# Kernel optimization log

Measured on AMD Instinct MI355X. Metric: run time of the kernel, lower is better.

Reference implementation:

```python
import jax, jax.numpy as jnp
import numpy as np

B, S, E, H = 32, 512, 512, 8
D = E // H  # head dim = 64
EPS = 1e-5


def setup_inputs() -> dict:
    key = jax.random.key(0)
    ks = jax.random.split(key, 6)
    x = jax.random.normal(ks[0], (B, S, E), dtype=jnp.float32)
    # nn.MultiheadAttention packed in-projection: [3E, E] weight, [3E] bias
    w_in = jax.random.normal(ks[1], (3 * E, E), dtype=jnp.float32) * 0.02
    b_in = jnp.zeros((3 * E,), dtype=jnp.float32)
    # out_proj: Linear(E, E)
    w_out = jax.random.normal(ks[2], (E, E), dtype=jnp.float32) * 0.02
    b_out = jnp.zeros((E,), dtype=jnp.float32)
    # LayerNorm(E) affine params
    gamma = jnp.ones((E,), dtype=jnp.float32)
    beta = jnp.zeros((E,), dtype=jnp.float32)
    return {"x": x, "w_in": w_in, "b_in": b_in, "w_out": w_out,
            "b_out": b_out, "gamma": gamma, "beta": beta}


def reference(x, w_in, b_in, w_out, b_out, gamma, beta):
    b, s, e = x.shape
    # packed QKV projection (torch: x @ W^T + b)
    qkv = x @ w_in.T + b_in                      # [B, S, 3E]
    q, k, v = jnp.split(qkv, 3, axis=-1)         # each [B, S, E]
    def to_heads(t):
        return t.reshape(b, s, H, D).transpose(0, 2, 1, 3)  # [B, H, S, D]
    q, k, v = to_heads(q), to_heads(k), to_heads(v)
    scores = jnp.einsum("bhqd,bhkd->bhqk", q, k) / jnp.sqrt(jnp.float32(D))
    att_w = jax.nn.softmax(scores, axis=-1)      # [B, H, S, S] per-head weights
    z = jnp.einsum("bhqk,bhkd->bhqd", att_w, v)  # [B, H, S, D]
    z = z.transpose(0, 2, 1, 3).reshape(b, s, e) # merge heads
    z = z @ w_out.T + b_out                      # out projection
    z = z + x                                    # residual connection
    # LayerNorm over last dim
    mu = jnp.mean(z, axis=-1, keepdims=True)
    var = jnp.var(z, axis=-1, keepdims=True)
    y = (z - mu) * jax.lax.rsqrt(var + EPS) * gamma + beta
    return (y, att_w)
```

## Files before the change

kernel.cpp:

```cpp
#include <hip/hip_runtime.h>
#include <hip/hip_bf16.h>
#include <stdint.h>

#define Bb 32
#define Ss 512
#define Ee 512
#define Hh 8
#define Dd 64
#define EPSf 1e-5f

typedef __attribute__((ext_vector_type(8))) unsigned short ushort8_t;
typedef __attribute__((ext_vector_type(4))) unsigned short ushort4_t;
typedef __attribute__((ext_vector_type(4))) float f32x4;
typedef __attribute__((ext_vector_type(4))) unsigned int uint4_t;
typedef __attribute__((ext_vector_type(8))) __bf16 bf16x8;

union U8cast { ushort8_t u; bf16x8 b; uint4_t w; };
__device__ __forceinline__ bf16x8 as_bf16x8(ushort8_t u) { U8cast c; c.u = u; return c.b; }
__device__ __forceinline__ bf16x8 words_bf16x8(unsigned int w0, unsigned int w1,
                                               unsigned int w2, unsigned int w3) {
  U8cast c; c.w = (uint4_t){w0, w1, w2, w3}; return c.b;
}

__device__ __forceinline__ unsigned short f2bf(float f) {
  __bf16 b = (__bf16)f;
  return __builtin_bit_cast(unsigned short, b);
}
__device__ __forceinline__ unsigned int pack2bf(float lo, float hi) {
  return ((unsigned int)f2bf(hi) << 16) | f2bf(lo);
}

__device__ __forceinline__ f32x4 mfma16(bf16x8 a, bf16x8 b, f32x4 c) {
  return __builtin_amdgcn_mfma_f32_16x16x32_bf16(a, b, c, 0, 0, 0);
}

__device__ __forceinline__ void async16(const unsigned short* g, unsigned short* l) {
  __builtin_amdgcn_global_load_lds(
      (const __attribute__((address_space(1))) void*)g,
      (__attribute__((address_space(3))) void*)l, 16, 0, 0);
}

__global__ __launch_bounds__(256) void cvt_all(
    const float* __restrict__ x, const float* __restrict__ win,
    const float* __restrict__ wout, unsigned short* __restrict__ dst) {
  const int NX = 1048576;
  const int NW = 98304;
  const int NT = NX + NW + 32768;
  int i = blockIdx.x * 256 + threadIdx.x;
  int stride = gridDim.x * 256;
  for (; i < NT; i += stride) {
    const float* s;
    int off;
    if (i < NX) { s = x; off = i; }
    else if (i < NX + NW) { s = win; off = i - NX; }
    else { s = wout; off = i - NX - NW; }
    float4 v0 = ((const float4*)s)[2 * off];
    float4 v1 = ((const float4*)s)[2 * off + 1];
    ushort8_t o;
    o[0] = f2bf(v0.x); o[1] = f2bf(v0.y); o[2] = f2bf(v0.z); o[3] = f2bf(v0.w);
    o[4] = f2bf(v1.x); o[5] = f2bf(v1.y); o[6] = f2bf(v1.z); o[7] = f2bf(v1.w);
    ((ushort8_t*)dst)[i] = o;
  }
}

__global__ __launch_bounds__(256) void qkv_mm(
    const unsigned short* __restrict__ Xb, const unsigned short* __restrict__ Wb,
    const float* __restrict__ bin,
    unsigned short* __restrict__ QL, unsigned short* __restrict__ KL,
    unsigned short* __restrict__ VL) {
  __shared__ unsigned short SH[128 * 128];
  unsigned short* As = SH;
  unsigned short* Bs = SH + 128 * 64;
  const int tid = threadIdx.x;
  const int w = tid >> 6, l = tid & 63;
  const int lr = l & 15, lg = l >> 4;
  const int id = blockIdx.x;
  const int gid = (id & 7) * 192 + (id >> 3);
  const int bx = gid % 12, by = gid / 12;
  const int m0 = by * 128, n0 = bx * 128;
  const int wm = (w >> 1) * 64, wn = (w & 1) * 64;
  f32x4 acc[4][4];
#pragma unroll
  for (int i = 0; i < 4; ++i)
#pragma unroll
    for (int j = 0; j < 4; ++j) acc[i][j] = (f32x4){0.f, 0.f, 0.f, 0.f};

  for (int k0 = 0; k0 < 512; k0 += 64) {
#pragma unroll
    for (int i = 0; i < 4; ++i) {
      int ci = (w * 4 + i) * 64 + l;
      int row = ci >> 3, kc = ci & 7;
      int gkc = kc ^ (row & 7);
      async16(Xb + (size_t)(m0 + row) * 512 + k0 + gkc * 8, &As[(w * 4 + i) * 512]);
      async16(Wb + (size_t)(n0 + row) * 512 + k0 + gkc * 8, &Bs[(w * 4 + i) * 512]);
    }
    __syncthreads();
#pragma unroll
    for (int ks = 0; ks < 2; ++ks) {
      bf16x8 af[4], bfr[4];
#pragma unroll
      for (int mf = 0; mf < 4; ++mf) {
        int row = wm + mf * 16 + lr;
        int gc = ks * 4 + lg;
        af[mf] = as_bf16x8(*(const ushort8_t*)&As[row * 64 + ((gc ^ (row & 7)) * 8)]);
      }
#pragma unroll
      for (int nf = 0; nf < 4; ++nf) {
        int row = wn + nf * 16 + lr;
        int gc = ks * 4 + lg;
        bfr[nf] = as_bf16x8(*(const ushort8_t*)&Bs[row * 64 + ((gc ^ (row & 7)) * 8)]);
      }
#pragma unroll
      for (int mf = 0; mf < 4; ++mf)
#pragma unroll
        for (int nf = 0; nf < 4; ++nf) acc[mf][nf] = mfma16(af[mf], bfr[nf], acc[mf][nf]);
    }
    __syncthreads();
  }

  const int which = n0 >> 9;
  const int bb = m0 >> 9, s0b = m0 & 511;
  const int h0 = (n0 & 511) >> 6;
#pragma unroll
  for (int nf = 0; nf < 4; ++nf) {
    int nl = wn + nf * 16 + lr;
    float bias = bin[n0 + nl];
#pragma unroll
    for (int mf = 0; mf < 4; ++mf) {
#pragma unroll
      for (int r = 0; r < 4; ++r) {
        int ml = wm + mf * 16 + lg * 4 + r;
        int row = (which == 2) ? nl : ml;
        int col = (which == 2) ? ml : nl;
        SH[row * 128 + ((((col >> 3) ^ (row & 7)) << 3) | (col & 7))] =
            f2bf(acc[mf][nf][r] + bias);
      }
    }
  }
  __syncthreads();

  unsigned short* dst = (which == 0) ? QL : (which == 1) ? KL : VL;
  const int frag0 = s0b >> 3;
#pragma unroll
  for (int i = 0; i < 8; ++i) {
    int c = tid + i * 256;
    int h_rel = c >> 10, cc = c & 1023;
    int fr = cc >> 6, ln = cc & 63;
    int row, col;
    if (which == 0) {
      row = (fr >> 1) * 16 + (ln & 15);
      col = h_rel * 64 + (fr & 1) * 32 + (ln >> 4) * 8;
    } else if (which == 1) {
      row = (fr >> 2) * 32 + ((fr >> 1) & 1) * 4 + ((ln & 15) >> 2) * 8 + (ln & 3);
      col = h_rel * 64 + (fr & 1) * 32 + (ln >> 4) * 8;
    } else {
      row = h_rel * 64 + (fr & 3) * 16 + (ln & 15);
      col = (fr >> 2) * 32 + (ln >> 4) * 8;
    }
    ushort8_t v = *(const ushort8_t*)&SH[row * 128 + (((col >> 3) ^ (row & 7)) << 3)];
    size_t base = (size_t)(bb * Hh + h0 + h_rel) * 32768;
    *(ushort8_t*)&dst[base + (size_t)(frag0 + fr) * 512 + ln * 8] = v;
  }
}

__global__ __launch_bounds__(512, 4) void attn_fused(
    const unsigned short* __restrict__ QL, const unsigned short* __restrict__ KL,
    const unsigned short* __restrict__ VL, float* __restrict__ att,
    unsigned short* __restrict__ Zb) {
  __shared__ unsigned short SH[2][8192];
  unsigned short* KB = &SH[0][0];
  const int tid = threadIdx.x;
  const int w = tid >> 6, l = tid & 63;
  const int lr = l & 15, lg = l >> 4;
  const int id = blockIdx.x;
  const int bh = (id >> 5) * 8 + (id & 7);
  const int m0 = ((id >> 3) & 3) * 128;
  const int b = bh >> 3, h = bh & 7;
  const unsigned short* Qp = QL + (size_t)bh * 32768;
  const unsigned short* Kp = KL + (size_t)bh * 32768;
  const unsigned short* Vp = VL + (size_t)bh * 32768;

  const int qb = (m0 >> 4) + w;
  bf16x8 bq0 = as_bf16x8(*(const ushort8_t*)(Qp + (size_t)(qb * 2) * 512 + l * 8));
  bf16x8 bq1 = as_bf16x8(*(const ushort8_t*)(Qp + (size_t)(qb * 2 + 1) * 512 + l * 8));

#define STAGE_K4(C)                                                            \
  async16(Kp + (size_t)(C)*4096 + w * 512 + l * 8,                             \
          &KB[((C) & 3) * 4096 + w * 512]);
#define STAGE_K(C, buf)                                                        \
  async16(Kp + (size_t)(C)*4096 + w * 512 + l * 8, &SH[buf][w * 512]);
#define STAGE_V(C, buf)                                                        \
  async16(Vp + (size_t)(C)*4096 + w * 512 + l * 8, &SH[buf][4096 + w * 512]);

  float ssum = 0.f;
  STAGE_K4(0);
  STAGE_K4(1);
  STAGE_K4(2);
#pragma unroll
  for (int C = 0; C < 8; ++C) {
    if (C <= 5) {
      asm volatile("s_waitcnt vmcnt(2)" ::: "memory");
    } else if (C == 6) {
      asm volatile("s_waitcnt vmcnt(1)" ::: "memory");
    } else {
      asm volatile("s_waitcnt vmcnt(0)" ::: "memory");
    }
    __builtin_amdgcn_s_barrier();
    if (C < 5) STAGE_K4(C + 3);
    f32x4 s4[4];
#pragma unroll
    for (int j = 0; j < 4; ++j) {
      bf16x8 ak0 = as_bf16x8(*(const ushort8_t*)&KB[(C & 3) * 4096 + (2 * j) * 512 + l * 8]);
      bf16x8 ak1 = as_bf16x8(*(const ushort8_t*)&KB[(C & 3) * 4096 + (2 * j + 1) * 512 + l * 8]);
      f32x4 z = (f32x4){0.f, 0.f, 0.f, 0.f};
      z = mfma16(ak0, bq0, z);
      s4[j] = mfma16(ak1, bq1, z);
    }
#pragma unroll
    for (int j = 0; j < 4; ++j) {
      float p0 = __expf(s4[j][0] * 0.125f);
      float p1 = __expf(s4[j][1] * 0.125f);
      float p2 = __expf(s4[j][2] * 0.125f);
      float p3 = __expf(s4[j][3] * 0.125f);
      ssum += (p0 + p1) + (p2 + p3);
    }
  }
  ssum += __shfl_xor(ssum, 16);
  ssum += __shfl_xor(ssum, 32);
  const float inv = 1.0f / ssum;
  __builtin_amdgcn_s_barrier();

  f32x4 o[4];
#pragma unroll
  for (int df = 0; df < 4; ++df) o[df] = (f32x4){0.f, 0.f, 0.f, 0.f};
  float* attb = att + (size_t)bh * Ss * Ss + (size_t)(m0 + w * 16) * Ss;
  const int dr8 = l >> 3, dc = l & 7;
  const int src0 = ((dc >> 1) << 4) + dr8;
  const int podd = dc & 1;

  STAGE_K(0, 0);
  STAGE_V(0, 0);
  __syncthreads();
#pragma unroll
  for (int C = 0; C < 8; ++C) {
    if (C < 7) {
      STAGE_K(C + 1, (C + 1) & 1);
      STAGE_V(C + 1, (C + 1) & 1);
    }
    f32x4 s4[4];
#pragma unroll
    for (int j = 0; j < 4; ++j) {
      bf16x8 ak0 = as_bf16x8(*(const ushort8_t*)&SH[C & 1][(2 * j) * 512 + l * 8]);
      bf16x8 ak1 = as_bf16x8(*(const ushort8_t*)&SH[C & 1][(2 * j + 1) * 512 + l * 8]);
      f32x4 z = (f32x4){0.f, 0.f, 0.f, 0.f};
      z = mfma16(ak0, bq0, z);
      s4[j] = mfma16(ak1, bq1, z);
    }
#pragma unroll
    for (int j = 0; j < 4; ++j)
#pragma unroll
      for (int r = 0; r < 4; ++r)
        s4[j][r] = __expf(s4[j][r] * 0.125f) * inv;

#pragma unroll
    for (int cc = 0; cc < 2; ++cc) {
      int c2 = 2 * C + cc;
#pragma unroll
      for (int hh = 0; hh < 2; ++hh) {
        int srcl = src0 + hh * 8;
        f32x4 g;
        g[0] = __shfl(s4[2 * cc + podd][0], srcl, 64);
        g[1] = __shfl(s4[2 * cc + podd][1], srcl, 64);
        g[2] = __shfl(s4[2 * cc + podd][2], srcl, 64);
        g[3] = __shfl(s4[2 * cc + podd][3], srcl, 64);
        float* p = attb + (size_t)(hh * 8 + dr8) * Ss + c2 * 32 + dc * 4;
        __builtin_nontemporal_store(g, (f32x4*)p);
      }
      bf16x8 bp = words_bf16x8(pack2bf(s4[2 * cc][0], s4[2 * cc][1]),
                               pack2bf(s4[2 * cc][2], s4[2 * cc][3]),
                               pack2bf(s4[2 * cc + 1][0], s4[2 * cc + 1][1]),
                               pack2bf(s4[2 * cc + 1][2], s4[2 * cc + 1][3]));
#pragma unroll
      for (int df = 0; df < 4; ++df) {
        bf16x8 av = as_bf16x8(
            *(const ushort8_t*)&SH[C & 1][4096 + (cc * 4 + df) * 512 + l * 8]);
        o[df] = mfma16(av, bp, o[df]);
      }
    }
    if (C < 7) {
      asm volatile("s_waitcnt vmcnt(4)" ::: "memory");
      __builtin_amdgcn_s_barrier();
    }
  }

  unsigned short* zrow = Zb + ((size_t)(b * Ss) + m0 + w * 16 + lr) * Ee + h * Dd;
#pragma unroll
  for (int df = 0; df < 4; ++df) {
    ushort4_t zz;
    zz[0] = f2bf(o[df][0]); zz[1] = f2bf(o[df][1]);
    zz[2] = f2bf(o[df][2]); zz[3] = f2bf(o[df][3]);
    *(ushort4_t*)(zrow + df * 16 + lg * 4) = zz;
  }
#undef STAGE_K4
#undef STAGE_K
#undef STAGE_V
}

__global__ __launch_bounds__(256) void out_ln(
    const unsigned short* __restrict__ Zb, const unsigned short* __restrict__ Wb,
    const float* __restrict__ bout, const float* __restrict__ X,
    const float* __restrict__ gamma, const float* __restrict__ beta,
    float* __restrict__ Y) {
  __shared__ unsigned short As[32 * 32];
  __shared__ unsigned short Bs[512 * 32];
  const int tid = threadIdx.x;
  const int w = tid >> 6, l = tid & 63;
  const int lr = l & 15, lg = l >> 4;
  const int id = blockIdx.x;
  const int gid = (id & 7) * 64 + (id >> 3);
  const int m0 = gid * 32;
  const int wn = w * 128;
  f32x4 acc[2][8];
#pragma unroll
  for (int i = 0; i < 2; ++i)
#pragma unroll
    for (int j = 0; j < 8; ++j) acc[i][j] = (f32x4){0.f, 0.f, 0.f, 0.f};

  for (int k0 = 0; k0 < 512; k0 += 32) {
#pragma unroll
    for (int i = 0; i < 8; ++i) {
      int ci = tid + i * 256;
      int row = ci >> 2, kc = ci & 3, gkc = kc ^ (row & 3);
      async16(Wb + (size_t)row * 512 + k0 + gkc * 8, &Bs[ci * 8]);
    }
    if (tid < 128) {
      int row = tid >> 2, kc = tid & 3, gkc = kc ^ (row & 3);
      async16(Zb + (size_t)(m0 + row) * 512 + k0 + gkc * 8, &As[tid * 8]);
    }
    __syncthreads();
    bf16x8 af[2], bfr[8];
#pragma unroll
    for (int mf = 0; mf < 2; ++mf) {
      int row = mf * 16 + lr;
      af[mf] = as_bf16x8(*(const ushort8_t*)&As[row * 32 + ((lg ^ (row & 3)) * 8)]);
    }
#pragma unroll
    for (int nf = 0; nf < 8; ++nf) {
      int row = wn + nf * 16 + lr;
      bfr[nf] = as_bf16x8(*(const ushort8_t*)&Bs[row * 32 + ((lg ^ (row & 3)) * 8)]);
    }
#pragma unroll
    for (int mf = 0; mf < 2; ++mf)
#pragma unroll
      for (int nf = 0; nf < 8; ++nf) acc[mf][nf] = mfma16(af[mf], bfr[nf], acc[mf][nf]);
    __syncthreads();
  }

  float sum[2][4], sq[2][4];
#pragma unroll
  for (int mf = 0; mf < 2; ++mf)
#pragma unroll
    for (int r = 0; r < 4; ++r) { sum[mf][r] = 0.f; sq[mf][r] = 0.f; }
#pragma unroll
  for (int nf = 0; nf < 8; ++nf) {
    int n = wn + nf * 16 + lr;
    float bias = bout[n];
#pragma unroll
    for (int mf = 0; mf < 2; ++mf)
#pragma unroll
      for (int r = 0; r < 4; ++r) {
        int m = m0 + mf * 16 + lg * 4 + r;
        float v = acc[mf][nf][r] + bias + X[(size_t)m * 512 + n];
        acc[mf][nf][r] = v;
        sum[mf][r] += v;
        sq[mf][r] += v * v;
      }
  }
#pragma unroll
  for (int mask = 1; mask < 16; mask <<= 1) {
#pragma unroll
    for (int mf = 0; mf < 2; ++mf)
#pragma unroll
      for (int r = 0; r < 4; ++r) {
        sum[mf][r] += __shfl_xor(sum[mf][r], mask);
        sq[mf][r] += __shfl_xor(sq[mf][r], mask);
      }
  }
  float* S = (float*)As;
  if (lr == 0) {
#pragma unroll
    for (int mf = 0; mf < 2; ++mf)
#pragma unroll
      for (int r = 0; r < 4; ++r) {
        int row = mf * 16 + lg * 4 + r;
        S[(w * 32 + row) * 2] = sum[mf][r];
        S[(w * 32 + row) * 2 + 1] = sq[mf][r];
      }
  }
  __syncthreads();
  float musv[2][4], rssv[2][4];
#pragma unroll
  for (int mf = 0; mf < 2; ++mf)
#pragma unroll
    for (int r = 0; r < 4; ++r) {
      int row = mf * 16 + lg * 4 + r;
      float t = 0.f, t2 = 0.f;
#pragma unroll
      for (int ww = 0; ww < 4; ++ww) {
        t += S[(ww * 32 + row) * 2];
        t2 += S[(ww * 32 + row) * 2 + 1];
      }
      float mu = t * (1.0f / 512.0f);
      float var = t2 * (1.0f / 512.0f) - mu * mu;
      musv[mf][r] = mu;
      rssv[mf][r] = rsqrtf(var + EPSf);
    }
#pragma unroll
  for (int nf = 0; nf < 8; ++nf) {
    int n = wn + nf * 16 + lr;
    float g = gamma[n], be = beta[n];
#pragma unroll
    for (int mf = 0; mf < 2; ++mf)
#pragma unroll
      for (int r = 0; r < 4; ++r) {
        int m = m0 + mf * 16 + lg * 4 + r;
        Y[(size_t)m * 512 + n] =
            (acc[mf][nf][r] - musv[mf][r]) * rssv[mf][r] * g + be;
      }
  }
}

extern "C" void kernel_launch(void* const* d_in, const int* in_sizes, int n_in,
                              void* d_out, int out_size, void* d_ws, size_t ws_size,
                              hipStream_t stream) {
  const float* x = (const float*)d_in[0];
  const float* w_in = (const float*)d_in[1];
  const float* b_in = (const float*)d_in[2];
  const float* w_out = (const float*)d_in[3];
  const float* b_out = (const float*)d_in[4];
  const float* gamma = (const float*)d_in[5];
  const float* beta = (const float*)d_in[6];

  float* y = (float*)d_out;
  float* att = (float*)d_out + (size_t)Bb * Ss * Ee;

  char* ws = (char*)d_ws;
  const size_t NBH = (size_t)Bb * Hh * Ss * Dd;
  unsigned short* QLb   = (unsigned short*)ws;
  unsigned short* KLb   = QLb + NBH;
  unsigned short* VLb   = KLb + NBH;
  unsigned short* xb    = VLb + NBH;
  unsigned short* Zb    = xb;
  unsigned short* winb  = xb + NBH;
  unsigned short* woutb = winb + (size_t)3 * Ee * Ee;

  cvt_all<<<dim3(2048), 256, 0, stream>>>(x, w_in, w_out, xb);
  qkv_mm<<<dim3(1536), 256, 0, stream>>>(xb, winb, b_in, QLb, KLb, VLb);
  attn_fused<<<dim3(1024), 512, 0, stream>>>(QLb, KLb, VLb, att, Zb);
  out_ln<<<dim3(512), 256, 0, stream>>>(Zb, woutb, b_out, x, gamma, beta, y);
}
```

Baseline: 156.5 us.

## Triple-buffer K/V staging in attention second pass with prefetch distance two

After: 154.3 us (median of 3 runs). No clear change (-1.4%).

```diff
diff --git a/kernel.cpp b/kernel.cpp
--- a/kernel.cpp
+++ b/kernel.cpp
@@ -167,8 +167,8 @@
     const unsigned short* __restrict__ QL, const unsigned short* __restrict__ KL,
     const unsigned short* __restrict__ VL, float* __restrict__ att,
     unsigned short* __restrict__ Zb) {
-  __shared__ unsigned short SH[2][8192];
-  unsigned short* KB = &SH[0][0];
+  __shared__ unsigned short SH3[3][8192];
+  unsigned short* KB = &SH3[0][0];
   const int tid = threadIdx.x;
   const int w = tid >> 6, l = tid & 63;
   const int lr = l & 15, lg = l >> 4;
@@ -187,10 +187,10 @@
 #define STAGE_K4(C)                                                            \
   async16(Kp + (size_t)(C)*4096 + w * 512 + l * 8,                             \
           &KB[((C) & 3) * 4096 + w * 512]);
-#define STAGE_K(C, buf)                                                        \
-  async16(Kp + (size_t)(C)*4096 + w * 512 + l * 8, &SH[buf][w * 512]);
-#define STAGE_V(C, buf)                                                        \
-  async16(Vp + (size_t)(C)*4096 + w * 512 + l * 8, &SH[buf][4096 + w * 512]);
+#define STAGE2_K(C, buf)                                                       \
+  async16(Kp + (size_t)(C)*4096 + w * 512 + l * 8, &SH3[buf][w * 512]);
+#define STAGE2_V(C, buf)                                                       \
+  async16(Vp + (size_t)(C)*4096 + w * 512 + l * 8, &SH3[buf][4096 + w * 512]);
 
   float ssum = 0.f;
   STAGE_K4(0);
@@ -238,20 +238,30 @@
   const int src0 = ((dc >> 1) << 4) + dr8;
   const int podd = dc & 1;
 
-  STAGE_K(0, 0);
-  STAGE_V(0, 0);
-  __syncthreads();
+  STAGE2_K(0, 0); STAGE2_V(0, 0);
+  STAGE2_K(1, 1); STAGE2_V(1, 1);
 #pragma unroll
   for (int C = 0; C < 8; ++C) {
-    if (C < 7) {
-      STAGE_K(C + 1, (C + 1) & 1);
-      STAGE_V(C + 1, (C + 1) & 1);
-    }
+    if (C == 0) {
+      asm volatile("s_waitcnt vmcnt(2)" ::: "memory");
+    } else if (C == 1) {
+      asm volatile("s_waitcnt vmcnt(6)" ::: "memory");
+    } else if (C < 7) {
+      asm volatile("s_waitcnt vmcnt(10)" ::: "memory");
+    } else {
+      asm volatile("s_waitcnt vmcnt(8)" ::: "memory");
+    }
+    __builtin_amdgcn_s_barrier();
+    if (C < 6) {
+      STAGE2_K(C + 2, (C + 2) % 3);
+      STAGE2_V(C + 2, (C + 2) % 3);
+    }
+    const int buf = C % 3;
     f32x4 s4[4];
 #pragma unroll
     for (int j = 0; j < 4; ++j) {
-      bf16x8 ak0 = as_bf16x8(*(const ushort8_t*)&SH[C & 1][(2 * j) * 512 + l * 8]);
-      bf16x8 ak1 = as_bf16x8(*(const ushort8_t*)&SH[C & 1][(2 * j + 1) * 512 + l * 8]);
+      bf16x8 ak0 = as_bf16x8(*(const ushort8_t*)&SH3[buf][(2 * j) * 512 + l * 8]);
+      bf16x8 ak1 = as_bf16x8(*(const ushort8_t*)&SH3[buf][(2 * j + 1) * 512 + l * 8]);
       f32x4 z = (f32x4){0.f, 0.f, 0.f, 0.f};
       z = mfma16(ak0, bq0, z);
       s4[j] = mfma16(ak1, bq1, z);
@@ -283,13 +293,9 @@
 #pragma unroll
       for (int df = 0; df < 4; ++df) {
         bf16x8 av = as_bf16x8(
-            *(const ushort8_t*)&SH[C & 1][4096 + (cc * 4 + df) * 512 + l * 8]);
+            *(const ushort8_t*)&SH3[buf][4096 + (cc * 4 + df) * 512 + l * 8]);
         o[df] = mfma16(av, bp, o[df]);
       }
-    }
-    if (C < 7) {
-      asm volatile("s_waitcnt vmcnt(4)" ::: "memory");
-      __builtin_amdgcn_s_barrier();
     }
   }
 
@@ -302,8 +308,8 @@
     *(ushort4_t*)(zrow + df * 16 + lg * 4) = zz;
   }
 #undef STAGE_K4
-#undef STAGE_K
-#undef STAGE_V
+#undef STAGE2_K
+#undef STAGE2_V
 }
 
 __global__ __launch_bounds__(256) void out_ln(
```

## Load full K and V per head into LDS once and loop over query tiles

Applied to the files above, without the earlier changes.

Result: slower. 415.5 us (+165.5%).

```diff
diff --git a/kernel.cpp b/kernel.cpp
--- a/kernel.cpp
+++ b/kernel.cpp
@@ -163,147 +163,124 @@
   }
 }
 
-__global__ __launch_bounds__(512, 4) void attn_fused(
+__global__ __launch_bounds__(512) void attn_fused(
     const unsigned short* __restrict__ QL, const unsigned short* __restrict__ KL,
     const unsigned short* __restrict__ VL, float* __restrict__ att,
     unsigned short* __restrict__ Zb) {
-  __shared__ unsigned short SH[2][8192];
-  unsigned short* KB = &SH[0][0];
+  __shared__ unsigned short KV[65536];
   const int tid = threadIdx.x;
   const int w = tid >> 6, l = tid & 63;
   const int lr = l & 15, lg = l >> 4;
-  const int id = blockIdx.x;
-  const int bh = (id >> 5) * 8 + (id & 7);
-  const int m0 = ((id >> 3) & 3) * 128;
+  const int bh = blockIdx.x;
   const int b = bh >> 3, h = bh & 7;
   const unsigned short* Qp = QL + (size_t)bh * 32768;
   const unsigned short* Kp = KL + (size_t)bh * 32768;
   const unsigned short* Vp = VL + (size_t)bh * 32768;
 
-  const int qb = (m0 >> 4) + w;
-  bf16x8 bq0 = as_bf16x8(*(const ushort8_t*)(Qp + (size_t)(qb * 2) * 512 + l * 8));
-  bf16x8 bq1 = as_bf16x8(*(const ushort8_t*)(Qp + (size_t)(qb * 2 + 1) * 512 + l * 8));
-
-#define STAGE_K4(C)                                                            \
-  async16(Kp + (size_t)(C)*4096 + w * 512 + l * 8,                             \
-          &KB[((C) & 3) * 4096 + w * 512]);
-#define STAGE_K(C, buf)                                                        \
-  async16(Kp + (size_t)(C)*4096 + w * 512 + l * 8, &SH[buf][w * 512]);
-#define STAGE_V(C, buf)                                                        \
-  async16(Vp + (size_t)(C)*4096 + w * 512 + l * 8, &SH[buf][4096 + w * 512]);
-
-  float ssum = 0.f;
-  STAGE_K4(0);
-  STAGE_K4(1);
-  STAGE_K4(2);
-#pragma unroll
-  for (int C = 0; C < 8; ++C) {
-    if (C <= 5) {
-      asm volatile("s_waitcnt vmcnt(2)" ::: "memory");
-    } else if (C == 6) {
-      asm volatile("s_waitcnt vmcnt(1)" ::: "memory");
-    } else {
-      asm volatile("s_waitcnt vmcnt(0)" ::: "memory");
-    }
-    __builtin_amdgcn_s_barrier();
-    if (C < 5) STAGE_K4(C + 3);
-    f32x4 s4[4];
-#pragma unroll
-    for (int j = 0; j < 4; ++j) {
-      bf16x8 ak0 = as_bf16x8(*(const ushort8_t*)&KB[(C & 3) * 4096 + (2 * j) * 512 + l * 8]);
-      bf16x8 ak1 = as_bf16x8(*(const ushort8_t*)&KB[(C & 3) * 4096 + (2 * j + 1) * 512 + l * 8]);
-      f32x4 z = (f32x4){0.f, 0.f, 0.f, 0.f};
-      z = mfma16(ak0, bq0, z);
-      s4[j] = mfma16(ak1, bq1, z);
-    }
-#pragma unroll
-    for (int j = 0; j < 4; ++j) {
-      float p0 = __expf(s4[j][0] * 0.125f);
-      float p1 = __expf(s4[j][1] * 0.125f);
-      float p2 = __expf(s4[j][2] * 0.125f);
-      float p3 = __expf(s4[j][3] * 0.125f);
-      ssum += (p0 + p1) + (p2 + p3);
-    }
-  }
-  ssum += __shfl_xor(ssum, 16);
-  ssum += __shfl_xor(ssum, 32);
-  const float inv = 1.0f / ssum;
-  __builtin_amdgcn_s_barrier();
-
-  f32x4 o[4];
-#pragma unroll
-  for (int df = 0; df < 4; ++df) o[df] = (f32x4){0.f, 0.f, 0.f, 0.f};
-  float* attb = att + (size_t)bh * Ss * Ss + (size_t)(m0 + w * 16) * Ss;
+#pragma unroll
+  for (int i = 0; i < 16; ++i) {
+    int j = i * 8 + w;
+    const unsigned short* src =
+        (j < 64) ? (Kp + (size_t)j * 512 + l * 8)
+                 : (Vp + (size_t)(j - 64) * 512 + l * 8);
+    async16(src, &KV[j * 512]);
+  }
+  __syncthreads();
+
   const int dr8 = l >> 3, dc = l & 7;
   const int src0 = ((dc >> 1) << 4) + dr8;
   const int podd = dc & 1;
 
-  STAGE_K(0, 0);
-  STAGE_V(0, 0);
-  __syncthreads();
-#pragma unroll
-  for (int C = 0; C < 8; ++C) {
-    if (C < 7) {
-      STAGE_K(C + 1, (C + 1) & 1);
-      STAGE_V(C + 1, (C + 1) & 1);
-    }
-    f32x4 s4[4];
-#pragma unroll
-    for (int j = 0; j < 4; ++j) {
-      bf16x8 ak0 = as_bf16x8(*(const ushort8_t*)&SH[C & 1][(2 * j) * 512 + l * 8]);
-      bf16x8 ak1 = as_bf16x8(*(const ushort8_t*)&SH[C & 1][(2 * j + 1) * 512 + l * 8]);
-      f32x4 z = (f32x4){0.f, 0.f, 0.f, 0.f};
-      z = mfma16(ak0, bq0, z);
-      s4[j] = mfma16(ak1, bq1, z);
-    }
-#pragma unroll
-    for (int j = 0; j < 4; ++j)
-#pragma unroll
-      for (int r = 0; r < 4; ++r)
-        s4[j][r] = __expf(s4[j][r] * 0.125f) * inv;
-
-#pragma unroll
-    for (int cc = 0; cc < 2; ++cc) {
-      int c2 = 2 * C + cc;
-#pragma unroll
-      for (int hh = 0; hh < 2; ++hh) {
-        int srcl = src0 + hh * 8;
-        f32x4 g;
-        g[0] = __shfl(s4[2 * cc + podd][0], srcl, 64);
-        g[1] = __shfl(s4[2 * cc + podd][1], srcl, 64);
-        g[2] = __shfl(s4[2 * cc + podd][2], srcl, 64);
-        g[3] = __shfl(s4[2 * cc + podd][3], srcl, 64);
-        float* p = attb + (size_t)(hh * 8 + dr8) * Ss + c2 * 32 + dc * 4;
-        __builtin_nontemporal_store(g, (f32x4*)p);
-      }
-      bf16x8 bp = words_bf16x8(pack2bf(s4[2 * cc][0], s4[2 * cc][1]),
-                               pack2bf(s4[2 * cc][2], s4[2 * cc][3]),
-                               pack2bf(s4[2 * cc + 1][0], s4[2 * cc + 1][1]),
-                               pack2bf(s4[2 * cc + 1][2], s4[2 * cc + 1][3]));
-#pragma unroll
-      for (int df = 0; df < 4; ++df) {
-        bf16x8 av = as_bf16x8(
-            *(const ushort8_t*)&SH[C & 1][4096 + (cc * 4 + df) * 512 + l * 8]);
-        o[df] = mfma16(av, bp, o[df]);
-      }
-    }
-    if (C < 7) {
-      asm volatile("s_waitcnt vmcnt(4)" ::: "memory");
-      __builtin_amdgcn_s_barrier();
-    }
-  }
-
-  unsigned short* zrow = Zb + ((size_t)(b * Ss) + m0 + w * 16 + lr) * Ee + h * Dd;
-#pragma unroll
-  for (int df = 0; df < 4; ++df) {
-    ushort4_t zz;
-    zz[0] = f2bf(o[df][0]); zz[1] = f2bf(o[df][1]);
-    zz[2] = f2bf(o[df][2]); zz[3] = f2bf(o[df][3]);
-    *(ushort4_t*)(zrow + df * 16 + lg * 4) = zz;
-  }
-#undef STAGE_K4
-#undef STAGE_K
-#undef STAGE_V
+  for (int p = 0; p < 4; ++p) {
+    const int m0 = p * 128;
+    const int qb = (m0 >> 4) + w;
+    bf16x8 bq0 = as_bf16x8(*(const ushort8_t*)(Qp + (size_t)(qb * 2) * 512 + l * 8));
+    bf16x8 bq1 = as_bf16x8(*(const ushort8_t*)(Qp + (size_t)(qb * 2 + 1) * 512 + l * 8));
+
+    float ssum = 0.f;
+#pragma unroll
+    for (int C = 0; C < 8; ++C) {
+      f32x4 s4[4];
+#pragma unroll
+      for (int j = 0; j < 4; ++j) {
+        int fr = 8 * C + 2 * j;
+        bf16x8 ak0 = as_bf16x8(*(const ushort8_t*)&KV[fr * 512 + l * 8]);
+        bf16x8 ak1 = as_bf16x8(*(const ushort8_t*)&KV[(fr + 1) * 512 + l * 8]);
+        f32x4 z = (f32x4){0.f, 0.f, 0.f, 0.f};
+        z = mfma16(ak0, bq0, z);
+        s4[j] = mfma16(ak1, bq1, z);
+      }
+#pragma unroll
+      for (int j = 0; j < 4; ++j) {
+        float p0 = __expf(s4[j][0] * 0.125f);
+        float p1 = __expf(s4[j][1] * 0.125f);
+        float p2 = __expf(s4[j][2] * 0.125f);
+        float p3 = __expf(s4[j][3] * 0.125f);
+        ssum += (p0 + p1) + (p2 + p3);
+      }
+    }
+    ssum += __shfl_xor(ssum, 16);
+    ssum += __shfl_xor(ssum, 32);
+    const float inv = 1.0f / ssum;
+
+    f32x4 o[4];
+#pragma unroll
+    for (int df = 0; df < 4; ++df) o[df] = (f32x4){0.f, 0.f, 0.f, 0.f};
+    float* attb = att + (size_t)bh * Ss * Ss + (size_t)(m0 + w * 16) * Ss;
+#pragma unroll
+    for (int C = 0; C < 8; ++C) {
+      f32x4 s4[4];
+#pragma unroll
+      for (int j = 0; j < 4; ++j) {
+        int fr = 8 * C + 2 * j;
+        bf16x8 ak0 = as_bf16x8(*(const ushort8_t*)&KV[fr * 512 + l * 8]);
+        bf16x8 ak1 = as_bf16x8(*(const ushort8_t*)&KV[(fr + 1) * 512 + l * 8]);
+        f32x4 z = (f32x4){0.f, 0.f, 0.f, 0.f};
+        z = mfma16(ak0, bq0, z);
+        s4[j] = mfma16(ak1, bq1, z);
+      }
+#pragma unroll
+      for (int j = 0; j < 4; ++j)
+#pragma unroll
+        for (int r = 0; r < 4; ++r)
+          s4[j][r] = __expf(s4[j][r] * 0.125f) * inv;
+
+#pragma unroll
+      for (int cc = 0; cc < 2; ++cc) {
+        int c2 = 2 * C + cc;
+#pragma unroll
+        for (int hh = 0; hh < 2; ++hh) {
+          int srcl = src0 + hh * 8;
+          f32x4 g;
+          g[0] = __shfl(s4[2 * cc + podd][0], srcl, 64);
+          g[1] = __shfl(s4[2 * cc + podd][1], srcl, 64);
+          g[2] = __shfl(s4[2 * cc + podd][2], srcl, 64);
+          g[3] = __shfl(s4[2 * cc + podd][3], srcl, 64);
+          float* pt = attb + (size_t)(hh * 8 + dr8) * Ss + c2 * 32 + dc * 4;
+          __builtin_nontemporal_store(g, (f32x4*)pt);
+        }
+        bf16x8 bp = words_bf16x8(pack2bf(s4[2 * cc][0], s4[2 * cc][1]),
+                                 pack2bf(s4[2 * cc][2], s4[2 * cc][3]),
+                                 pack2bf(s4[2 * cc + 1][0], s4[2 * cc + 1][1]),
+                                 pack2bf(s4[2 * cc + 1][2], s4[2 * cc + 1][3]));
+#pragma unroll
+        for (int df = 0; df < 4; ++df) {
+          bf16x8 av = as_bf16x8(
+              *(const ushort8_t*)&KV[32768 + (c2 * 4 + df) * 512 + l * 8]);
+          o[df] = mfma16(av, bp, o[df]);
+        }
+      }
+    }
+
+    unsigned short* zrow = Zb + ((size_t)(b * Ss) + m0 + w * 16 + lr) * Ee + h * Dd;
+#pragma unroll
+    for (int df = 0; df < 4; ++df) {
+      ushort4_t zz;
+      zz[0] = f2bf(o[df][0]); zz[1] = f2bf(o[df][1]);
+      zz[2] = f2bf(o[df][2]); zz[3] = f2bf(o[df][3]);
+      *(ushort4_t*)(zrow + df * 16 + lg * 4) = zz;
+    }
+  }
 }
 
 __global__ __launch_bounds__(256) void out_ln(
@@ -456,6 +433,6 @@
 
   cvt_all<<<dim3(2048), 256, 0, stream>>>(x, w_in, w_out, xb);
   qkv_mm<<<dim3(1536), 256, 0, stream>>>(xb, winb, b_in, QLb, KLb, VLb);
-  attn_fused<<<dim3(1024), 512, 0, stream>>>(QLb, KLb, VLb, att, Zb);
+  attn_fused<<<dim3(256), 512, 0, stream>>>(QLb, KLb, VLb, att, Zb);
   out_ln<<<dim3(512), 256, 0, stream>>>(Zb, woutb, b_out, x, gamma, beta, y);
 }
```
